# Optimization experiments

Measured on AMD Instinct MI355X. Metric: run time of the kernel, lower is better.

Reference implementation:

```python
import jax, jax.numpy as jnp
import numpy as np

S, B, D, DOUT = 512, 32, 1024, 1024


def setup_inputs() -> dict:
    key = jax.random.key(0)
    ks = jax.random.split(key, 7)
    scale = 1.0 / np.sqrt(D)
    return {
        "x": jax.random.normal(ks[0], (S, B, D), dtype=jnp.float32),
        "w1_w": jax.random.normal(ks[1], (D, D), dtype=jnp.float32) * scale,
        "w1_b": jax.random.normal(ks[2], (D,), dtype=jnp.float32) * scale,
        "w2_w": jax.random.normal(ks[3], (DOUT, D), dtype=jnp.float32) * scale,
        "w2_b": jax.random.normal(ks[4], (DOUT,), dtype=jnp.float32) * scale,
        "model_w": jax.random.normal(ks[5], (DOUT, D), dtype=jnp.float32) * scale,
        "model_b": jax.random.normal(ks[6], (DOUT,), dtype=jnp.float32) * scale,
    }


def reference(x, w1_w, w1_b, w2_w, w2_b, model_w, model_b):
    # x: [S, B, D]; gating vectors from the first token of each sequence
    x0 = x[0]                                   # [B, D]
    v1 = x0 @ w1_w.T + w1_b                     # [B, D]
    v2 = x0 @ w2_w.T + w2_b                     # [B, DOUT]
    # rank-1 outer product gate, sigmoid, elementwise-modulated weight
    mask = jax.nn.sigmoid(v1[:, :, None] * v2[:, None, :])  # [B, D, DOUT]
    mask = mask * model_w.T                     # [B, D, DOUT]
    out = jnp.einsum('sbd,bdf->sbf', x, mask) + model_b      # [S, B, DOUT]
    return out
```

## Files before the change

### kernel.cpp

```cpp
#include <hip/hip_runtime.h>
#include <hip/hip_bf16.h>

#define S_ 512
#define B_ 32
#define D_ 1024
#define F_ 1024

typedef float f32x4 __attribute__((ext_vector_type(4)));
typedef short bf16x8 __attribute__((ext_vector_type(8)));

__device__ __forceinline__ unsigned short f2bf(float f) {
    __hip_bfloat16 h = __float2bfloat16(f);
    return *reinterpret_cast<unsigned short*>(&h);
}

__device__ __forceinline__ float sigmoidf_fast(float x) {
    float e = __builtin_amdgcn_exp2f(x * -1.44269504088896f);
    return __builtin_amdgcn_rcpf(1.0f + e);
}

__global__ __launch_bounds__(256) void vker(
    const float* __restrict__ x,
    const float* __restrict__ w1w, const float* __restrict__ w1b,
    const float* __restrict__ w2w, const float* __restrict__ w2b,
    float* __restrict__ vbuf)
{
    __shared__ float xs[B_][132];
    __shared__ float wst[64][132];
    int fb = blockIdx.x & 31;
    int ks = blockIdx.x >> 5;
    int k0 = ks * 128;
    int t  = threadIdx.x;
    const float* w = (fb < 16) ? w1w : w2w;
    int fbase = (fb < 16) ? fb * 64 : (fb - 16) * 64;

    #pragma unroll
    for (int i = 0; i < 4; ++i) {
        int q = t + 256 * i;
        int row = q >> 5, c4 = (q & 31) * 4;
        float4 v = *reinterpret_cast<const float4*>(x + (size_t)row * D_ + k0 + c4);
        *reinterpret_cast<float4*>(&xs[row][c4]) = v;
    }
    #pragma unroll
    for (int i = 0; i < 8; ++i) {
        int q = t + 256 * i;
        int row = q >> 5, c4 = (q & 31) * 4;
        float4 v = *reinterpret_cast<const float4*>(w + (size_t)(fbase + row) * D_ + k0 + c4);
        *reinterpret_cast<float4*>(&wst[row][c4]) = v;
    }
    __syncthreads();

    int b   = t >> 3;
    int fl0 = t & 7;
    float acc[8] = {0,0,0,0,0,0,0,0};
    for (int k4 = 0; k4 < 32; ++k4) {
        float4 xv = *reinterpret_cast<const float4*>(&xs[b][k4 * 4]);
        #pragma unroll
        for (int j = 0; j < 8; ++j) {
            float4 wv = *reinterpret_cast<const float4*>(&wst[fl0 + 8 * j][k4 * 4]);
            acc[j] += xv.x * wv.x + xv.y * wv.y + xv.z * wv.z + xv.w * wv.w;
        }
    }
    #pragma unroll
    for (int j = 0; j < 8; ++j) {
        int fg = fb * 64 + fl0 + 8 * j;
        float v = acc[j];
        if (ks == 0) v += (fg < 1024) ? w1b[fg] : w2b[fg - 1024];
        atomicAdd(&vbuf[b * 2048 + fg], v);
    }
}

#define BM 128
#define BN 128
#define BK 64
#define LDA 72

__global__ __launch_bounds__(256) void gemm(
    const float* __restrict__ x,
    const float* __restrict__ mw, const float* __restrict__ mb,
    const float* __restrict__ vbuf,
    float* __restrict__ out)
{
    __shared__ __hip_bfloat16 As[BM * LDA];
    __shared__ __hip_bfloat16 Bs[BN * LDA];
    __shared__ float v2s[BN];

    int bid = blockIdx.x;
    int b   = bid >> 5;
    int t32 = bid & 31;
    int mt  = t32 & 3;
    int nt  = t32 >> 2;
    int s0 = mt * BM, n0 = nt * BN;

    int tid  = threadIdx.x;
    int lane = tid & 63, wid = tid >> 6;
    int wr = (wid >> 1) * 64;
    int wc = (wid & 1) * 64;

    if (tid < BN) v2s[tid] = vbuf[b * 2048 + 1024 + n0 + tid];

    f32x4 acc[4][4] = {};

    const size_t xb = (size_t)b * D_;
    for (int kt = 0; kt < D_ / BK; ++kt) {
        int k0 = kt * BK;
        __syncthreads();
        #pragma unroll
        for (int i = 0; i < 8; ++i) {
            int q = tid + 256 * i;
            int row = q >> 4;
            int c = (q & 15) * 4;
            float4 v = *reinterpret_cast<const float4*>(
                x + (size_t)(s0 + row) * (B_ * D_) + xb + k0 + c);
            unsigned long long pk =
                  (unsigned long long)f2bf(v.x)
                | ((unsigned long long)f2bf(v.y) << 16)
                | ((unsigned long long)f2bf(v.z) << 32)
                | ((unsigned long long)f2bf(v.w) << 48);
            *reinterpret_cast<unsigned long long*>(&As[row * LDA + c]) = pk;
        }
        #pragma unroll
        for (int i = 0; i < 8; ++i) {
            int q = tid + 256 * i;
            int n = q >> 4;
            int c = (q & 15) * 4;
            float4 wv = *reinterpret_cast<const float4*>(mw + (size_t)(n0 + n) * D_ + k0 + c);
            float4 v1 = *reinterpret_cast<const float4*>(vbuf + b * 2048 + k0 + c);
            float v2  = v2s[n];
            unsigned long long pk =
                  (unsigned long long)f2bf(sigmoidf_fast(v1.x * v2) * wv.x)
                | ((unsigned long long)f2bf(sigmoidf_fast(v1.y * v2) * wv.y) << 16)
                | ((unsigned long long)f2bf(sigmoidf_fast(v1.z * v2) * wv.z) << 32)
                | ((unsigned long long)f2bf(sigmoidf_fast(v1.w * v2) * wv.w) << 48);
            *reinterpret_cast<unsigned long long*>(&Bs[n * LDA + c]) = pk;
        }
        __syncthreads();
        #pragma unroll
        for (int kh = 0; kh < 2; ++kh) {
            int ko = (lane >> 4) * 8 + kh * 32;
            bf16x8 af[4], bfr[4];
            #pragma unroll
            for (int m2 = 0; m2 < 4; ++m2)
                af[m2] = *reinterpret_cast<const bf16x8*>(
                    &As[(wr + m2 * 16 + (lane & 15)) * LDA + ko]);
            #pragma unroll
            for (int n2 = 0; n2 < 4; ++n2)
                bfr[n2] = *reinterpret_cast<const bf16x8*>(
                    &Bs[(wc + n2 * 16 + (lane & 15)) * LDA + ko]);
            #pragma unroll
            for (int m2 = 0; m2 < 4; ++m2)
                #pragma unroll
                for (int n2 = 0; n2 < 4; ++n2)
                    acc[m2][n2] = __builtin_amdgcn_mfma_f32_16x16x32_bf16(
                        af[m2], bfr[n2], acc[m2][n2], 0, 0, 0);
        }
    }

    int col = lane & 15, rg = (lane >> 4) * 4;
    float bias[4];
    #pragma unroll
    for (int n2 = 0; n2 < 4; ++n2) bias[n2] = mb[n0 + wc + n2 * 16 + col];
    #pragma unroll
    for (int m2 = 0; m2 < 4; ++m2) {
        #pragma unroll
        for (int n2 = 0; n2 < 4; ++n2) {
            #pragma unroll
            for (int r = 0; r < 4; ++r) {
                int srow = s0 + wr + m2 * 16 + rg + r;
                out[(size_t)srow * (B_ * F_) + b * F_ + n0 + wc + n2 * 16 + col]
                    = acc[m2][n2][r] + bias[n2];
            }
        }
    }
}

extern "C" void kernel_launch(void* const* d_in, const int* in_sizes, int n_in,
                              void* d_out, int out_size, void* d_ws, size_t ws_size,
                              hipStream_t stream) {
    const float* x   = (const float*)d_in[0];
    const float* w1w = (const float*)d_in[1];
    const float* w1b = (const float*)d_in[2];
    const float* w2w = (const float*)d_in[3];
    const float* w2b = (const float*)d_in[4];
    const float* mw  = (const float*)d_in[5];
    const float* mb  = (const float*)d_in[6];
    float* vbuf = (float*)d_ws;
    float* outp = (float*)d_out;

    hipMemsetAsync(vbuf, 0, B_ * 2048 * sizeof(float), stream);
    vker<<<256, 256, 0, stream>>>(x, w1w, w1b, w2w, w2b, vbuf);
    gemm<<<32 * 4 * 8, 256, 0, stream>>>(x, mw, mb, vbuf, outp);
}
```

Baseline: 227.3 us.

## Precompute bf16 activations and per-batch masked weights before a DMA-fed GEMM

Splits the fused GEMM into three kernels. One converts x to bf16 in a [B,S,D] layout, one materializes the sigmoid-gated masked weight per batch as bf16, and a GEMM then streams both into LDS with global_load_lds direct loads. The goal is to remove the redundant per-tile sigmoid and conversion work, which was repeated for every M tile, and to simplify the GEMM's load path. In exchange it adds about 96MB of workspace traffic and two extra launches. If the workspace is too small it falls back to the old fused kernel.

Result: no change. 227.5 us (+0.1%).

```diff
diff --git a/kernel.cpp b/kernel.cpp
--- a/kernel.cpp
+++ b/kernel.cpp
@@ -70,40 +70,152 @@
     }
 }
 
-#define BM 128
-#define BN 128
-#define BK 64
-#define LDA 72
-
-__global__ __launch_bounds__(256) void gemm(
-    const float* __restrict__ x,
-    const float* __restrict__ mw, const float* __restrict__ mb,
-    const float* __restrict__ vbuf,
+__global__ __launch_bounds__(256) void xcvt(
+    const float* __restrict__ x, unsigned short* __restrict__ xb)
+{
+    int g = blockIdx.x * 256 + threadIdx.x;
+    size_t base = (size_t)g * 8;
+    int d  = (int)(base & 1023);
+    int sb = (int)(base >> 10);
+    int b = sb & 31, s = sb >> 5;
+    float4 a = *reinterpret_cast<const float4*>(x + base);
+    float4 c = *reinterpret_cast<const float4*>(x + base + 4);
+    union { unsigned short u[8]; bf16x8 v; } p;
+    p.u[0] = f2bf(a.x); p.u[1] = f2bf(a.y); p.u[2] = f2bf(a.z); p.u[3] = f2bf(a.w);
+    p.u[4] = f2bf(c.x); p.u[5] = f2bf(c.y); p.u[6] = f2bf(c.z); p.u[7] = f2bf(c.w);
+    *reinterpret_cast<bf16x8*>(xb + ((size_t)(b * S_ + s) * D_ + d)) = p.v;
+}
+
+__global__ __launch_bounds__(256) void maskgen(
+    const float* __restrict__ mw, const float* __restrict__ vbuf,
+    unsigned short* __restrict__ mbf)
+{
+    int b  = blockIdx.x & 31;
+    int fc = blockIdx.x >> 5;
+    int t  = threadIdx.x;
+    float4 v1 = *reinterpret_cast<const float4*>(vbuf + b * 2048 + t * 4);
+    const float* v2p = vbuf + b * 2048 + 1024 + fc * 16;
+    #pragma unroll 4
+    for (int r = 0; r < 16; ++r) {
+        int f = fc * 16 + r;
+        float v2 = v2p[r];
+        float4 w = *reinterpret_cast<const float4*>(mw + (size_t)f * D_ + t * 4);
+        ushort4 p;
+        p.x = f2bf(sigmoidf_fast(v1.x * v2) * w.x);
+        p.y = f2bf(sigmoidf_fast(v1.y * v2) * w.y);
+        p.z = f2bf(sigmoidf_fast(v1.z * v2) * w.z);
+        p.w = f2bf(sigmoidf_fast(v1.w * v2) * w.w);
+        *reinterpret_cast<ushort4*>(mbf + ((size_t)(b * F_ + f) * D_ + t * 4)) = p;
+    }
+}
+
+__global__ __launch_bounds__(256) void gemm_bf(
+    const unsigned short* __restrict__ xb,
+    const unsigned short* __restrict__ mbf,
+    const float* __restrict__ mb,
     float* __restrict__ out)
 {
-    __shared__ __hip_bfloat16 As[BM * LDA];
-    __shared__ __hip_bfloat16 Bs[BN * LDA];
-    __shared__ float v2s[BN];
+    __shared__ __align__(16) unsigned short As[128 * 64];
+    __shared__ __align__(16) unsigned short Bs[128 * 64];
 
     int bid = blockIdx.x;
     int b   = bid >> 5;
     int t32 = bid & 31;
     int mt  = t32 & 3;
     int nt  = t32 >> 2;
-    int s0 = mt * BM, n0 = nt * BN;
+    int s0 = mt * 128, n0 = nt * 128;
+
+    int tid = threadIdx.x, lane = tid & 63, wid = tid >> 6;
+    int wr = (wid >> 1) * 64, wc = (wid & 1) * 64;
+
+    int lrow = lane >> 3;
+    int lcol = (lane & 7) * 8;
+    const unsigned short* ag = xb  + ((size_t)(b * S_ + s0) * D_) + lcol;
+    const unsigned short* bg = mbf + ((size_t)(b * F_ + n0) * D_) + lcol;
+
+    f32x4 acc[4][4] = {};
+    for (int kt = 0; kt < 16; ++kt) {
+        int k0 = kt * 64;
+        __syncthreads();
+        #pragma unroll
+        for (int i = 0; i < 4; ++i) {
+            int rr = (wid * 4 + i) * 8 + lrow;
+            __builtin_amdgcn_global_load_lds(
+                (const __attribute__((address_space(1))) void*)(ag + (size_t)rr * D_ + k0),
+                (__attribute__((address_space(3))) void*)(As + (wid * 4 + i) * 512),
+                16, 0, 0);
+            __builtin_amdgcn_global_load_lds(
+                (const __attribute__((address_space(1))) void*)(bg + (size_t)rr * D_ + k0),
+                (__attribute__((address_space(3))) void*)(Bs + (wid * 4 + i) * 512),
+                16, 0, 0);
+        }
+        __syncthreads();
+        #pragma unroll
+        for (int kh = 0; kh < 2; ++kh) {
+            int ko = (lane >> 4) * 8 + kh * 32;
+            bf16x8 af[4], bfr[4];
+            #pragma unroll
+            for (int m2 = 0; m2 < 4; ++m2)
+                af[m2] = *reinterpret_cast<const bf16x8*>(
+                    &As[(wr + m2 * 16 + (lane & 15)) * 64 + ko]);
+            #pragma unroll
+            for (int n2 = 0; n2 < 4; ++n2)
+                bfr[n2] = *reinterpret_cast<const bf16x8*>(
+                    &Bs[(wc + n2 * 16 + (lane & 15)) * 64 + ko]);
+            #pragma unroll
+            for (int m2 = 0; m2 < 4; ++m2)
+                #pragma unroll
+                for (int n2 = 0; n2 < 4; ++n2)
+                    acc[m2][n2] = __builtin_amdgcn_mfma_f32_16x16x32_bf16(
+                        af[m2], bfr[n2], acc[m2][n2], 0, 0, 0);
+        }
+    }
+
+    int col = lane & 15, rg = (lane >> 4) * 4;
+    float bias[4];
+    #pragma unroll
+    for (int n2 = 0; n2 < 4; ++n2) bias[n2] = mb[n0 + wc + n2 * 16 + col];
+    #pragma unroll
+    for (int m2 = 0; m2 < 4; ++m2)
+        #pragma unroll
+        for (int n2 = 0; n2 < 4; ++n2)
+            #pragma unroll
+            for (int r = 0; r < 4; ++r) {
+                int srow = s0 + wr + m2 * 16 + rg + r;
+                out[(size_t)srow * (B_ * F_) + b * F_ + n0 + wc + n2 * 16 + col]
+                    = acc[m2][n2][r] + bias[n2];
+            }
+}
+
+#define LDA 72
+__global__ __launch_bounds__(256) void gemm_fused(
+    const float* __restrict__ x,
+    const float* __restrict__ mw, const float* __restrict__ mb,
+    const float* __restrict__ vbuf,
+    float* __restrict__ out)
+{
+    __shared__ __hip_bfloat16 As[128 * LDA];
+    __shared__ __hip_bfloat16 Bs[128 * LDA];
+    __shared__ float v2s[128];
+
+    int bid = blockIdx.x;
+    int b   = bid >> 5;
+    int t32 = bid & 31;
+    int mt  = t32 & 3;
+    int nt  = t32 >> 2;
+    int s0 = mt * 128, n0 = nt * 128;
 
     int tid  = threadIdx.x;
     int lane = tid & 63, wid = tid >> 6;
     int wr = (wid >> 1) * 64;
     int wc = (wid & 1) * 64;
 
-    if (tid < BN) v2s[tid] = vbuf[b * 2048 + 1024 + n0 + tid];
+    if (tid < 128) v2s[tid] = vbuf[b * 2048 + 1024 + n0 + tid];
 
     f32x4 acc[4][4] = {};
-
-    const size_t xb = (size_t)b * D_;
-    for (int kt = 0; kt < D_ / BK; ++kt) {
-        int k0 = kt * BK;
+    const size_t xbo = (size_t)b * D_;
+    for (int kt = 0; kt < 16; ++kt) {
+        int k0 = kt * 64;
         __syncthreads();
         #pragma unroll
         for (int i = 0; i < 8; ++i) {
@@ -111,7 +223,7 @@
             int row = q >> 4;
             int c = (q & 15) * 4;
             float4 v = *reinterpret_cast<const float4*>(
-                x + (size_t)(s0 + row) * (B_ * D_) + xb + k0 + c);
+                x + (size_t)(s0 + row) * (B_ * D_) + xbo + k0 + c);
             unsigned long long pk =
                   (unsigned long long)f2bf(v.x)
                 | ((unsigned long long)f2bf(v.y) << 16)
@@ -161,17 +273,15 @@
     #pragma unroll
     for (int n2 = 0; n2 < 4; ++n2) bias[n2] = mb[n0 + wc + n2 * 16 + col];
     #pragma unroll
-    for (int m2 = 0; m2 < 4; ++m2) {
-        #pragma unroll
-        for (int n2 = 0; n2 < 4; ++n2) {
+    for (int m2 = 0; m2 < 4; ++m2)
+        #pragma unroll
+        for (int n2 = 0; n2 < 4; ++n2)
             #pragma unroll
             for (int r = 0; r < 4; ++r) {
                 int srow = s0 + wr + m2 * 16 + rg + r;
                 out[(size_t)srow * (B_ * F_) + b * F_ + n0 + wc + n2 * 16 + col]
                     = acc[m2][n2][r] + bias[n2];
             }
-        }
-    }
 }
 
 extern "C" void kernel_launch(void* const* d_in, const int* in_sizes, int n_in,
@@ -184,10 +294,20 @@
     const float* w2b = (const float*)d_in[4];
     const float* mw  = (const float*)d_in[5];
     const float* mb  = (const float*)d_in[6];
+    float* outp = (float*)d_out;
+
     float* vbuf = (float*)d_ws;
-    float* outp = (float*)d_out;
+    unsigned short* xb  = (unsigned short*)((char*)d_ws + ((size_t)1 << 20));
+    unsigned short* mbf = (unsigned short*)((char*)d_ws + ((size_t)33 << 20));
+    size_t need = (size_t)97 << 20;
 
     hipMemsetAsync(vbuf, 0, B_ * 2048 * sizeof(float), stream);
     vker<<<256, 256, 0, stream>>>(x, w1w, w1b, w2w, w2b, vbuf);
-    gemm<<<32 * 4 * 8, 256, 0, stream>>>(x, mw, mb, vbuf, outp);
-}
+    if (ws_size >= need) {
+        xcvt<<<8192, 256, 0, stream>>>(x, xb);
+        maskgen<<<2048, 256, 0, stream>>>(mw, vbuf, mbf);
+        gemm_bf<<<1024, 256, 0, stream>>>(xb, mbf, mb, outp);
+    } else {
+        gemm_fused<<<1024, 256, 0, stream>>>(x, mw, mb, vbuf, outp);
+    }
+}
```

## Restructure gated GEMM with register prefetch, swizzled LDS and larger tiles

Applied to the files above, without the earlier changes.

Replaces the 128x128 GEMM kernel with a 512-thread kernel that computes 256x128 output tiles. While the MFMA loop runs on the current K tile, it holds the next tile's global loads of x, model_w and v1 in registers, so global latency overlaps compute. The padded LDS rows become XOR-swizzled 64-element rows, and the block index is remapped so consecutive blocks share the same weight tile across batches. In exchange it uses more registers per thread and launches fewer, larger blocks, which can lower occupancy.

Result: slower. 256.2 us (+12.7%).

```diff
diff --git a/kernel.cpp b/kernel.cpp
--- a/kernel.cpp
+++ b/kernel.cpp
@@ -9,12 +9,12 @@
 typedef float f32x4 __attribute__((ext_vector_type(4)));
 typedef short bf16x8 __attribute__((ext_vector_type(8)));
 
-__device__ __forceinline__ unsigned short f2bf(float f) {
+static __device__ __forceinline__ unsigned short f2bf(float f) {
     __hip_bfloat16 h = __float2bfloat16(f);
     return *reinterpret_cast<unsigned short*>(&h);
 }
 
-__device__ __forceinline__ float sigmoidf_fast(float x) {
+static __device__ __forceinline__ float sigmoidf_fast(float x) {
     float e = __builtin_amdgcn_exp2f(x * -1.44269504088896f);
     return __builtin_amdgcn_rcpf(1.0f + e);
 }
@@ -70,108 +70,129 @@
     }
 }
 
-#define BM 128
-#define BN 128
-#define BK 64
-#define LDA 72
-
-__global__ __launch_bounds__(256) void gemm(
-    const float* __restrict__ x,
-    const float* __restrict__ mw, const float* __restrict__ mb,
-    const float* __restrict__ vbuf,
+__global__ __launch_bounds__(512) void fused(
+    const float* __restrict__ x, const float* __restrict__ mw,
+    const float* __restrict__ mb, const float* __restrict__ vbuf,
     float* __restrict__ out)
 {
-    __shared__ __hip_bfloat16 As[BM * LDA];
-    __shared__ __hip_bfloat16 Bs[BN * LDA];
-    __shared__ float v2s[BN];
-
-    int bid = blockIdx.x;
-    int b   = bid >> 5;
-    int t32 = bid & 31;
-    int mt  = t32 & 3;
-    int nt  = t32 >> 2;
-    int s0 = mt * BM, n0 = nt * BN;
-
-    int tid  = threadIdx.x;
-    int lane = tid & 63, wid = tid >> 6;
-    int wr = (wid >> 1) * 64;
-    int wc = (wid & 1) * 64;
-
-    if (tid < BN) v2s[tid] = vbuf[b * 2048 + 1024 + n0 + tid];
+    __shared__ __align__(16) unsigned short As[256 * 64];
+    __shared__ __align__(16) unsigned short Bs[128 * 64];
+    __shared__ float v2s[128];
+
+    const int bid = blockIdx.x;
+    const int b   = (bid & 7) + ((bid >> 3) & 3) * 8;
+    const int rem = bid >> 5;
+    const int f0  = (rem & 7) * 128;
+    const int s0  = (rem >> 3) * 256;
+
+    const int tid  = threadIdx.x;
+    const int lane = tid & 63, wid = tid >> 6;
+    const int wr = (wid >> 1) * 64;
+    const int wc = (wid & 1) * 64;
+
+    if (tid < 128) v2s[tid] = vbuf[b * 2048 + 1024 + f0 + tid];
+
+    const int arow = tid >> 1;
+    const int adc  = (tid & 1) * 32;
+    const float* ap = x + (size_t)(s0 + arow) * (B_ * D_) + (size_t)b * D_ + adc;
+    const int brow = tid >> 2;
+    const int bdc  = (tid & 3) * 16;
+    const float* wp = mw + (size_t)(f0 + brow) * D_ + bdc;
+    const float* vp = vbuf + b * 2048 + bdc;
+
+    unsigned short* Abase = As + arow * 64;
+    unsigned short* Bbase = Bs + brow * 64;
+    const int aswz = arow & 7, bswz = brow & 7;
+    const int acb  = adc >> 3;
+    const int bcb  = bdc >> 3;
 
     f32x4 acc[4][4] = {};
-
-    const size_t xb = (size_t)b * D_;
-    for (int kt = 0; kt < D_ / BK; ++kt) {
-        int k0 = kt * BK;
-        __syncthreads();
-        #pragma unroll
-        for (int i = 0; i < 8; ++i) {
-            int q = tid + 256 * i;
-            int row = q >> 4;
-            int c = (q & 15) * 4;
-            float4 v = *reinterpret_cast<const float4*>(
-                x + (size_t)(s0 + row) * (B_ * D_) + xb + k0 + c);
-            unsigned long long pk =
-                  (unsigned long long)f2bf(v.x)
-                | ((unsigned long long)f2bf(v.y) << 16)
-                | ((unsigned long long)f2bf(v.z) << 32)
-                | ((unsigned long long)f2bf(v.w) << 48);
-            *reinterpret_cast<unsigned long long*>(&As[row * LDA + c]) = pk;
-        }
-        #pragma unroll
-        for (int i = 0; i < 8; ++i) {
-            int q = tid + 256 * i;
-            int n = q >> 4;
-            int c = (q & 15) * 4;
-            float4 wv = *reinterpret_cast<const float4*>(mw + (size_t)(n0 + n) * D_ + k0 + c);
-            float4 v1 = *reinterpret_cast<const float4*>(vbuf + b * 2048 + k0 + c);
-            float v2  = v2s[n];
-            unsigned long long pk =
-                  (unsigned long long)f2bf(sigmoidf_fast(v1.x * v2) * wv.x)
-                | ((unsigned long long)f2bf(sigmoidf_fast(v1.y * v2) * wv.y) << 16)
-                | ((unsigned long long)f2bf(sigmoidf_fast(v1.z * v2) * wv.z) << 32)
-                | ((unsigned long long)f2bf(sigmoidf_fast(v1.w * v2) * wv.w) << 48);
-            *reinterpret_cast<unsigned long long*>(&Bs[n * LDA + c]) = pk;
-        }
-        __syncthreads();
+    float4 av[8], wv[4], v1v[4];
+
+#define LOADS(K0) do { \
+    _Pragma("unroll") for (int i = 0; i < 8; ++i) \
+        av[i] = *reinterpret_cast<const float4*>(ap + (K0) + i * 4); \
+    _Pragma("unroll") for (int i = 0; i < 4; ++i) { \
+        wv[i]  = *reinterpret_cast<const float4*>(wp + (K0) + i * 4); \
+        v1v[i] = *reinterpret_cast<const float4*>(vp + (K0) + i * 4); } \
+} while (0)
+
+    LOADS(0);
+    asm volatile("s_waitcnt lgkmcnt(0)" ::: "memory");
+
+    for (int kt = 0; kt < 16; ++kt) {
+        __builtin_amdgcn_s_barrier();
+        #pragma unroll
+        for (int j = 0; j < 4; ++j) {
+            union { unsigned short u[8]; bf16x8 v; } p;
+            float4 lo = av[2 * j], hi = av[2 * j + 1];
+            p.u[0] = f2bf(lo.x); p.u[1] = f2bf(lo.y);
+            p.u[2] = f2bf(lo.z); p.u[3] = f2bf(lo.w);
+            p.u[4] = f2bf(hi.x); p.u[5] = f2bf(hi.y);
+            p.u[6] = f2bf(hi.z); p.u[7] = f2bf(hi.w);
+            *reinterpret_cast<bf16x8*>(Abase + (((acb + j) ^ aswz) << 3)) = p.v;
+        }
+        {
+            float v2 = v2s[brow];
+            #pragma unroll
+            for (int j = 0; j < 2; ++j) {
+                union { unsigned short u[8]; bf16x8 v; } p;
+                float4 va = v1v[2 * j], vb = v1v[2 * j + 1];
+                float4 wa = wv[2 * j],  wb = wv[2 * j + 1];
+                p.u[0] = f2bf(sigmoidf_fast(va.x * v2) * wa.x);
+                p.u[1] = f2bf(sigmoidf_fast(va.y * v2) * wa.y);
+                p.u[2] = f2bf(sigmoidf_fast(va.z * v2) * wa.z);
+                p.u[3] = f2bf(sigmoidf_fast(va.w * v2) * wa.w);
+                p.u[4] = f2bf(sigmoidf_fast(vb.x * v2) * wb.x);
+                p.u[5] = f2bf(sigmoidf_fast(vb.y * v2) * wb.y);
+                p.u[6] = f2bf(sigmoidf_fast(vb.z * v2) * wb.z);
+                p.u[7] = f2bf(sigmoidf_fast(vb.w * v2) * wb.w);
+                *reinterpret_cast<bf16x8*>(Bbase + (((bcb + j) ^ bswz) << 3)) = p.v;
+            }
+        }
+        if (kt < 15) LOADS((kt + 1) * 64);
+        asm volatile("s_waitcnt lgkmcnt(0)" ::: "memory");
+        __builtin_amdgcn_s_barrier();
         #pragma unroll
         for (int kh = 0; kh < 2; ++kh) {
-            int ko = (lane >> 4) * 8 + kh * 32;
-            bf16x8 af[4], bfr[4];
-            #pragma unroll
-            for (int m2 = 0; m2 < 4; ++m2)
+            const int kslot = (lane >> 4) + kh * 4;
+            bf16x8 af[4], bq[4];
+            #pragma unroll
+            for (int m2 = 0; m2 < 4; ++m2) {
+                int r = wr + m2 * 16 + (lane & 15);
                 af[m2] = *reinterpret_cast<const bf16x8*>(
-                    &As[(wr + m2 * 16 + (lane & 15)) * LDA + ko]);
-            #pragma unroll
-            for (int n2 = 0; n2 < 4; ++n2)
-                bfr[n2] = *reinterpret_cast<const bf16x8*>(
-                    &Bs[(wc + n2 * 16 + (lane & 15)) * LDA + ko]);
+                    As + r * 64 + ((kslot ^ (r & 7)) << 3));
+            }
+            #pragma unroll
+            for (int n2 = 0; n2 < 4; ++n2) {
+                int r = wc + n2 * 16 + (lane & 15);
+                bq[n2] = *reinterpret_cast<const bf16x8*>(
+                    Bs + r * 64 + ((kslot ^ (r & 7)) << 3));
+            }
             #pragma unroll
             for (int m2 = 0; m2 < 4; ++m2)
                 #pragma unroll
                 for (int n2 = 0; n2 < 4; ++n2)
                     acc[m2][n2] = __builtin_amdgcn_mfma_f32_16x16x32_bf16(
-                        af[m2], bfr[n2], acc[m2][n2], 0, 0, 0);
-        }
-    }
-
-    int col = lane & 15, rg = (lane >> 4) * 4;
+                        af[m2], bq[n2], acc[m2][n2], 0, 0, 0);
+        }
+    }
+#undef LOADS
+
+    const int col = lane & 15, rg = (lane >> 4) * 4;
     float bias[4];
     #pragma unroll
-    for (int n2 = 0; n2 < 4; ++n2) bias[n2] = mb[n0 + wc + n2 * 16 + col];
-    #pragma unroll
-    for (int m2 = 0; m2 < 4; ++m2) {
-        #pragma unroll
-        for (int n2 = 0; n2 < 4; ++n2) {
+    for (int n2 = 0; n2 < 4; ++n2) bias[n2] = mb[f0 + wc + n2 * 16 + col];
+    #pragma unroll
+    for (int m2 = 0; m2 < 4; ++m2)
+        #pragma unroll
+        for (int n2 = 0; n2 < 4; ++n2)
             #pragma unroll
             for (int r = 0; r < 4; ++r) {
                 int srow = s0 + wr + m2 * 16 + rg + r;
-                out[(size_t)srow * (B_ * F_) + b * F_ + n0 + wc + n2 * 16 + col]
+                out[(size_t)srow * (B_ * F_) + b * F_ + f0 + wc + n2 * 16 + col]
                     = acc[m2][n2][r] + bias[n2];
             }
-        }
-    }
 }
 
 extern "C" void kernel_launch(void* const* d_in, const int* in_sizes, int n_in,
@@ -184,10 +205,10 @@
     const float* w2b = (const float*)d_in[4];
     const float* mw  = (const float*)d_in[5];
     const float* mb  = (const float*)d_in[6];
+    float* outp = (float*)d_out;
     float* vbuf = (float*)d_ws;
-    float* outp = (float*)d_out;
 
     hipMemsetAsync(vbuf, 0, B_ * 2048 * sizeof(float), stream);
     vker<<<256, 256, 0, stream>>>(x, w1w, w1b, w2w, w2b, vbuf);
-    gemm<<<32 * 4 * 8, 256, 0, stream>>>(x, mw, mb, vbuf, outp);
-}
+    fused<<<512, 512, 0, stream>>>(x, mw, mb, vbuf, outp);
+}
```
